# Kernel tuning notes

Hardware: AMD Instinct MI355X
Metric: run time of the kernel (lower is better)

Reference implementation:

```python
import jax, jax.numpy as jnp
import numpy as np

MOLS = 64
ATOMS = 256
N = MOLS * ATOMS
K_GB = 32
K_GNN = 16
HID = 128
OFFSET = 0.009            # GB dielectric offset (nm)
ALPHA, BETA, GAMMA = 1.0, 0.8, 4.85  # OBC2 coefficients
EPS_FACTOR = 138.935456   # Coulomb constant, kJ*nm/(mol*e^2)
PREF = -EPS_FACTOR * (1.0 - 1.0 / 78.5)


def _edges(key, k_neigh):
    # random intra-molecule neighbors, no self loops (mimics radius-graph structure)
    src = jnp.repeat(jnp.arange(N), k_neigh)
    off = jax.random.randint(key, (N * k_neigh,), 1, ATOMS)
    dst = (src // ATOMS) * ATOMS + (src % ATOMS + off) % ATOMS
    return jnp.stack([src, dst]).astype(jnp.int32)


def setup_inputs() -> dict:
    key = jax.random.key(0)
    ks = jax.random.split(key, 8)
    pos = (jax.random.uniform(ks[0], (N, 3), jnp.float32) * 1.5)
    q = jax.random.uniform(ks[1], (N, 1), jnp.float32) - 0.5
    rad = 0.15 + 0.05 * jax.random.uniform(ks[2], (N, 1), jnp.float32)
    scl = 0.8 + 0.2 * jax.random.uniform(ks[3], (N, 1), jnp.float32)
    rest = jax.random.uniform(ks[4], (N, 4), jnp.float32)
    atom_features = jnp.concatenate([q, rad, scl, rest], axis=1)
    batch = jnp.repeat(jnp.arange(MOLS), ATOMS).astype(jnp.int32)
    edge_index = _edges(ks[5], K_GB)
    gnn_edge_index = _edges(ks[6], K_GNN)

    def lin(k, fi, fo):
        return (jax.random.normal(k, (fi, fo), jnp.float32) / np.float32(np.sqrt(fi)),
                jnp.zeros((fo,), jnp.float32))
    kw = jax.random.split(ks[7], 6)
    i1_w1, i1_b1 = lin(kw[0], 2 * 2 + 1, HID)
    i1_w2, i1_b2 = lin(kw[1], HID, HID)
    i2_w1, i2_b1 = lin(kw[2], 2 * HID + 1, HID)
    i2_w2, i2_b2 = lin(kw[3], HID, HID)
    i3_w1, i3_b1 = lin(kw[4], 2 * HID + 1, HID)
    i3_w2, i3_b2 = lin(kw[5], HID, 1)
    return dict(pos=pos, atom_features=atom_features, batch=batch,
                edge_index=edge_index, gnn_edge_index=gnn_edge_index,
                i1_w1=i1_w1, i1_b1=i1_b1, i1_w2=i1_w2, i1_b2=i1_b2,
                i2_w1=i2_w1, i2_b1=i2_b1, i2_w2=i2_w2, i2_b2=i2_b2,
                i3_w1=i3_w1, i3_b1=i3_b1, i3_w2=i3_w2, i3_b2=i3_b2)


def _dist(pos, ei):
    d2 = jnp.sum((pos[ei[0]] - pos[ei[1]]) ** 2, axis=1)
    return jnp.sqrt(d2 + 1e-12)


def _gb_energies(pos, feats, ei):
    # GBNeck_interaction (Born radii via HCT descreening integral, OBC2 rescale)
    # followed by GBNeck_energies (pairwise GB + self energy), per-atom [N,1]
    n = pos.shape[0]
    src, dst = ei[0], ei[1]
    d = _dist(pos, ei)
    q, radius, scale = feats[:, 0], feats[:, 1], feats[:, 2]
    rho = radius - OFFSET
    sr_j = (scale * rho)[src]
    rho_i = rho[dst]
    U = d + sr_j
    L = jnp.maximum(rho_i, jnp.abs(d - sr_j))
    I = 0.5 * (1.0 / L - 1.0 / U
               + 0.25 * (d - sr_j ** 2 / d) * (1.0 / U ** 2 - 1.0 / L ** 2)
               + 0.5 * jnp.log(L / U) / d)
    I = jnp.where(rho_i < U, I, 0.0)
    Isum = jax.ops.segment_sum(I, dst, num_segments=n)
    psi = Isum * rho
    B = 1.0 / (1.0 / rho - jnp.tanh(ALPHA * psi - BETA * psi ** 2 + GAMMA * psi ** 3) / radius)
    Bi, Bj = B[dst], B[src]
    f_gb = jnp.sqrt(d ** 2 + Bi * Bj * jnp.exp(-d ** 2 / (4.0 * Bi * Bj)))
    e_pair = 0.5 * PREF * q[dst] * q[src] / f_gb  # 0.5: edges are double counted
    e = 0.5 * PREF * q ** 2 / B + jax.ops.segment_sum(e_pair, dst, num_segments=n)
    return e[:, None]


def _in_layer(x, ei, d, w1, b1, w2, b2):
    # IN_layer_all_swish_2pass: edge MLP on [x_i || x_j || d] + scatter-add
    n = x.shape[0]
    m = jnp.concatenate([x[ei[0]], x[ei[1]], d[:, None]], axis=1)
    h = jax.nn.silu(m @ w1 + b1)
    return jax.ops.segment_sum(h @ w2 + b2, ei[1], num_segments=n)


def _energies_all(pos, feats, ei, gei,
                  i1_w1, i1_b1, i1_w2, i1_b2,
                  i2_w1, i2_b1, i2_w2, i2_b2,
                  i3_w1, i3_b1, i3_w2, i3_b2):
    e_gb = _gb_energies(pos, feats, ei)
    d_gnn = _dist(pos, gei)
    x = jax.nn.silu(_in_layer(feats[:, :2], gei, d_gnn, i1_w1, i1_b1, i1_w2, i1_b2))
    x = jax.nn.silu(_in_layer(x, gei, d_gnn, i2_w1, i2_b1, i2_w2, i2_b2))
    x = _in_layer(x, gei, d_gnn, i3_w1, i3_b1, i3_w2, i3_b2)
    return e_gb + x


def reference(pos, atom_features, batch, edge_index, gnn_edge_index,
              i1_w1, i1_b1, i1_w2, i1_b2,
              i2_w1, i2_b1, i2_w2, i2_b2,
              i3_w1, i3_b1, i3_w2, i3_b2):
    ws = (i1_w1, i1_b1, i1_w2, i1_b2, i2_w1, i2_b1, i2_w2, i2_b2,
          i3_w1, i3_b1, i3_w2, i3_b2)
    efun = lambda p: _energies_all(p, atom_features, edge_index, gnn_edge_index, *ws)
    energies, vjp = jax.vjp(efun, pos)  # [N,1]
    (gpos,) = vjp(jnp.ones_like(energies))
    forces = -gpos
    energy = jax.ops.segment_sum(energies[:, 0], batch, num_segments=MOLS)[:, None]
    return energy, forces
```

## Files before the change

### kernel.cpp

```cpp
#include <hip/hip_runtime.h>
#include <hip/hip_bf16.h>

#define NATOMS 16384
#define MOLS   64
#define ATOMSM 256
#define EGB    524288
#define EGNN   262144
#define HID    128
#define NH     (NATOMS*HID)

#define OFFSETC 0.009f
#define ALPHAC  1.0f
#define BETAC   0.8f
#define GAMMAC  4.85f
#define PREFC   (-138.935456f*(1.0f-1.0f/78.5f))

typedef __hip_bfloat16 bf;
typedef __attribute__((ext_vector_type(8))) short bf8v;
typedef __attribute__((ext_vector_type(4))) float f4v;

__device__ __forceinline__ float b2f(bf x){ return __bfloat162float(x); }
__device__ __forceinline__ bf f2b(float x){ return __float2bfloat16(x); }
__device__ __forceinline__ short f2s(float x){ bf h = f2b(x); return *(short*)&h; }
__device__ __forceinline__ float s2f(short s){
    unsigned int x = ((unsigned int)(unsigned short)s) << 16;
    return __uint_as_float(x);
}
__device__ __forceinline__ float sigf(float x){ return 1.0f/(1.0f+__expf(-x)); }
__device__ __forceinline__ float waveRed(float v){
    v += __shfl_xor(v,32); v += __shfl_xor(v,16); v += __shfl_xor(v,8);
    v += __shfl_xor(v,4);  v += __shfl_xor(v,2);  v += __shfl_xor(v,1);
    return v;
}

__global__ __launch_bounds__(256) void k_gbA_dist(
    const float* __restrict__ pos, const float* __restrict__ feat,
    const int* __restrict__ ei, float* __restrict__ Isum,
    const int* __restrict__ gei, float* __restrict__ dgnn, int* __restrict__ cnt)
{
    int tid = threadIdx.x;
    if (blockIdx.x < 512){
        __shared__ float sPx[256], sPy[256], sPz[256], sRho[256], sSr[256];
        __shared__ float sI[256];
        int mbase = (blockIdx.x >> 3) * 256;
        {
            int i = mbase + tid;
            sPx[tid]=pos[3*i]; sPy[tid]=pos[3*i+1]; sPz[tid]=pos[3*i+2];
            float rad = feat[7*i+1], sc = feat[7*i+2];
            float rho = rad - OFFSETC;
            sRho[tid]=rho; sSr[tid]=sc*rho;
            sI[tid]=0.f;
        }
        __syncthreads();
        int T = blockIdx.x*256 + tid;
        int s = T >> 3, p = T & 7;
        int sl = s & 255;
        int e0 = s*32 + p*4;
        float px = sPx[sl], py = sPy[sl], pz = sPz[sl];
        float sr = sSr[sl];
        const int* dP = ei + EGB;
#pragma unroll
        for (int j=0;j<4;j++){
            int dl = dP[e0+j] & 255;
            float dx = px - sPx[dl];
            float dy = py - sPy[dl];
            float dz = pz - sPz[dl];
            float d  = sqrtf(dx*dx+dy*dy+dz*dz + 1e-12f);
            float rho_i = sRho[dl];
            float U = d + sr;
            if (rho_i < U){
                float L = fmaxf(rho_i, fabsf(d - sr));
                float invU = 1.0f/U, invL = 1.0f/L;
                float I = 0.5f*invL - 0.5f*invU
                        + 0.125f*(d - sr*sr/d)*(invU*invU - invL*invL)
                        + 0.25f*__logf(L*invU)/d;
                atomicAdd(&sI[dl], I);
            }
        }
        __syncthreads();
        atomicAdd(&Isum[mbase + tid], sI[tid]);
    } else {
        int e = (blockIdx.x-512)*256 + tid;
        if (e >= EGNN) return;
        int s = gei[e], dd = gei[EGNN+e];
        float dx = pos[3*s+0] - pos[3*dd+0];
        float dy = pos[3*s+1] - pos[3*dd+1];
        float dz = pos[3*s+2] - pos[3*dd+2];
        dgnn[e] = sqrtf(dx*dx+dy*dy+dz*dz + 1e-12f);
        atomicAdd(&cnt[dd], 1);
    }
}

__global__ __launch_bounds__(256) void k_gbB_scan(
    const float* __restrict__ feat, const float* __restrict__ Isum,
    float* __restrict__ Bv, float* __restrict__ cB, float* __restrict__ gB,
    float* __restrict__ egb,
    const int* __restrict__ cnt, int* __restrict__ rptr, int* __restrict__ cursor)
{
    int t = threadIdx.x;
    if (blockIdx.x < 64){
        int i = blockIdx.x*256 + t;
        float q   = feat[7*i+0];
        float rad = feat[7*i+1];
        float rho = rad - OFFSETC;
        float psi = Isum[i]*rho;
        float u = psi*(ALPHAC + psi*(-BETAC + GAMMAC*psi));
        float tt = tanhf(u);
        float B = 1.0f/(1.0f/rho - tt/rad);
        Bv[i] = B;
        float du = ALPHAC + psi*(-2.0f*BETAC + 3.0f*GAMMAC*psi);
        cB[i] = B*B*((1.0f-tt*tt)/rad)*du*rho;
        float Cs = 0.5f*PREFC*q*q;
        egb[i] = Cs/B;
        gB[i]  = -Cs/(B*B);
    } else {
        __shared__ int sc[256];
        int m = blockIdx.x - 64;
        int c = cnt[m*256+t];
        sc[t] = c; __syncthreads();
        for (int off=1; off<256; off<<=1){
            int x = (t>=off) ? sc[t-off] : 0;
            __syncthreads();
            sc[t] += x;
            __syncthreads();
        }
        int ex = m*4096 + sc[t] - c;
        rptr[m*256+t] = ex;
        cursor[m*256+t] = ex;
    }
}

__global__ __launch_bounds__(256) void k_gbC(
    const float* __restrict__ pos, const float* __restrict__ feat,
    const int* __restrict__ ei, const float* __restrict__ Bv,
    float* __restrict__ egb, float* __restrict__ gdgb, float* __restrict__ gB)
{
    __shared__ float sPx[256], sPy[256], sPz[256], sB[256], sQf[256];
    __shared__ float sE[256], sG[256];
    int tid = threadIdx.x;
    int mbase = (blockIdx.x >> 3) * 256;
    {
        int i = mbase + tid;
        sPx[tid]=pos[3*i]; sPy[tid]=pos[3*i+1]; sPz[tid]=pos[3*i+2];
        sB[tid]=Bv[i]; sQf[tid]=feat[7*i+0];
        sE[tid]=0.f; sG[tid]=0.f;
    }
    __syncthreads();
    int T = blockIdx.x*256 + tid;
    int s = T >> 3, p = T & 7;
    int sl = s & 255;
    int e0 = s*32 + p*4;
    float px = sPx[sl], py = sPy[sl], pz = sPz[sl];
    float qs = sQf[sl];
    float Bs = sB[sl];
    float gsrc = 0.f;
    const int* dP = ei + EGB;
#pragma unroll
    for (int j=0;j<4;j++){
        int dl = dP[e0+j] & 255;
        float dx = px - sPx[dl];
        float dy = py - sPy[dl];
        float dz = pz - sPz[dl];
        float d2 = dx*dx+dy*dy+dz*dz + 1e-12f;
        float d  = sqrtf(d2);
        float Bd = sB[dl];
        float C = 0.5f*PREFC*sQf[dl]*qs;
        float P = Bd*Bs;
        float ex = __expf(-d2/(4.f*P));
        float f2 = d2 + P*ex;
        float f  = sqrtf(f2);
        float f3i = 1.f/(f2*f);
        gdgb[e0+j] = -C*d*(1.f - 0.25f*ex)*f3i;
        float common = -C*ex*(1.f + d2/(4.f*P))*0.5f*f3i;
        atomicAdd(&sE[dl], C/f);
        atomicAdd(&sG[dl], common*Bs);
        gsrc += common*Bd;
    }
    gsrc += __shfl_xor(gsrc,1);
    gsrc += __shfl_xor(gsrc,2);
    gsrc += __shfl_xor(gsrc,4);
    if (p==0) atomicAdd(&sG[sl], gsrc);
    __syncthreads();
    atomicAdd(&egb[mbase + tid], sE[tid]);
    atomicAdd(&gB[mbase + tid],  sG[tid]);
}

__global__ __launch_bounds__(256) void k_gbE(
    const float* __restrict__ pos, const float* __restrict__ feat,
    const int* __restrict__ ei, const float* __restrict__ cB,
    const float* __restrict__ gB,
    const float* __restrict__ gdgb, float* __restrict__ grad)
{
    __shared__ float sPx[256], sPy[256], sPz[256], sRho[256], sSr[256], sCg[256];
    __shared__ float sGx[256], sGy[256], sGz[256];
    int tid = threadIdx.x;
    int mbase = (blockIdx.x >> 3) * 256;
    {
        int i = mbase + tid;
        sPx[tid]=pos[3*i]; sPy[tid]=pos[3*i+1]; sPz[tid]=pos[3*i+2];
        float rad = feat[7*i+1], sc = feat[7*i+2];
        float rho = rad - OFFSETC;
        sRho[tid]=rho; sSr[tid]=sc*rho;
        sCg[tid]=cB[i]*gB[i];
        sGx[tid]=0.f; sGy[tid]=0.f; sGz[tid]=0.f;
    }
    __syncthreads();
    int T = blockIdx.x*256 + tid;
    int s = T >> 3, p = T & 7;
    int sl = s & 255;
    int e0 = s*32 + p*4;
    float px = sPx[sl], py = sPy[sl], pz = sPz[sl];
    float sr = sSr[sl];
    float gx=0.f, gy=0.f, gz=0.f;
    const int* dP = ei + EGB;
#pragma unroll
    for (int j=0;j<4;j++){
        int dl = dP[e0+j] & 255;
        float dx = px - sPx[dl];
        float dy = py - sPy[dl];
        float dz = pz - sPz[dl];
        float d2 = dx*dx+dy*dy+dz*dz + 1e-12f;
        float d  = sqrtf(d2);
        float rho_i = sRho[dl];
        float U = d + sr;
        float gd = gdgb[e0+j];
        if (rho_i < U){
            float aa = fabsf(d - sr);
            float L, Lp;
            if (rho_i >= aa){ L = rho_i; Lp = 0.f; }
            else { L = aa; Lp = (d >= sr) ? 1.f : -1.f; }
            float invU = 1.f/U, invL = 1.f/L;
            float invU2=invU*invU, invL2=invL*invL;
            float dIdd = -0.5f*Lp*invL2 + 0.5f*invU2
                + 0.125f*(1.f + sr*sr/d2)*(invU2 - invL2)
                + 0.125f*(d - sr*sr/d)*(2.f*Lp*invL2*invL - 2.f*invU2*invU)
                + 0.25f*((Lp*invL - invU)/d - __logf(L*invU)/d2);
            gd += sCg[dl]*dIdd;
        }
        float c = gd/d;
        gx += c*dx; gy += c*dy; gz += c*dz;
        atomicAdd(&sGx[dl], -c*dx);
        atomicAdd(&sGy[dl], -c*dy);
        atomicAdd(&sGz[dl], -c*dz);
    }
    gx += __shfl_xor(gx,1); gx += __shfl_xor(gx,2); gx += __shfl_xor(gx,4);
    gy += __shfl_xor(gy,1); gy += __shfl_xor(gy,2); gy += __shfl_xor(gy,4);
    gz += __shfl_xor(gz,1); gz += __shfl_xor(gz,2); gz += __shfl_xor(gz,4);
    if (p==0){
        atomicAdd(&sGx[sl], gx);
        atomicAdd(&sGy[sl], gy);
        atomicAdd(&sGz[sl], gz);
    }
    __syncthreads();
    int i = mbase + tid;
    atomicAdd(&grad[3*i+0], sGx[tid]);
    atomicAdd(&grad[3*i+1], sGy[tid]);
    atomicAdd(&grad[3*i+2], sGz[tid]);
}

__global__ __launch_bounds__(256) void k_fill(
    const int* __restrict__ gei, int* __restrict__ cursor, int* __restrict__ csr)
{
    int e = blockIdx.x*256 + threadIdx.x;
    if (e >= EGNN) return;
    int dst = gei[EGNN+e];
    int pos = atomicAdd(&cursor[dst], 1);
    csr[pos] = e;
}

__global__ __launch_bounds__(256) void k_pre(
    const float* __restrict__ A2, const float* __restrict__ C1,
    const float* __restrict__ A3, const float* __restrict__ C2,
    short* __restrict__ C1t, short* __restrict__ C2t,
    short* __restrict__ A2at, short* __restrict__ A2bt,
    short* __restrict__ A3at, short* __restrict__ A3bt,
    short* __restrict__ rA2a, short* __restrict__ rA2b,
    short* __restrict__ rA3a, short* __restrict__ rA3b,
    short* __restrict__ rC1, short* __restrict__ rC2,
    const float* __restrict__ feat, const float* __restrict__ A1,
    bf* __restrict__ u1, bf* __restrict__ v1)
{
    if (blockIdx.x < 64){
        int gid = blockIdx.x*256 + threadIdx.x;
        int j = gid >> 7, k = gid & 127;
        C1t[gid]  = f2s(C1[k*HID+j]);
        C2t[gid]  = f2s(C2[k*HID+j]);
        A2at[gid] = f2s(A2[k*HID+j]);
        A2bt[gid] = f2s(A2[(HID+k)*HID+j]);
        A3at[gid] = f2s(A3[k*HID+j]);
        A3bt[gid] = f2s(A3[(HID+k)*HID+j]);
        rA2a[gid] = f2s(A2[gid]);
        rA2b[gid] = f2s(A2[HID*HID+gid]);
        rA3a[gid] = f2s(A3[gid]);
        rA3b[gid] = f2s(A3[HID*HID+gid]);
        rC1[gid]  = f2s(C1[gid]);
        rC2[gid]  = f2s(C2[gid]);
    } else {
        int gid = (blockIdx.x-64)*256 + threadIdx.x;
        int i = gid >> 7, k = gid & 127;
        float q = feat[7*i+0], r = feat[7*i+1];
        u1[gid] = f2b(q*A1[k]       + r*A1[HID+k]);
        v1[gid] = f2b(q*A1[2*HID+k] + r*A1[3*HID+k]);
    }
}

__global__ __launch_bounds__(128) void k_edge_fwd_dst(
    const int* __restrict__ csr, const int* __restrict__ rptr, const int* __restrict__ cnt,
    const float* __restrict__ dgnn, const bf* __restrict__ u, const bf* __restrict__ v,
    const float* __restrict__ wdp, const float* __restrict__ bb,
    bf* __restrict__ Hs, bf* __restrict__ dsO, bf* __restrict__ Sds)
{
    int dst = blockIdx.x, k = threadIdx.x;
    int n = cnt[dst], r0 = rptr[dst];
    float wd = wdp[k];
    float base = b2f(v[dst*HID+k]) + bb[k];
    float hsum = 0.f, dssum = 0.f;
    const short* us = (const short*)u;
    short* dso = (short*)dsO;
#pragma unroll 2
    for (int j=0;j<n;j++){
        int e = csr[r0+j];
        float a = s2f(us[(size_t)(e>>4)*HID + k]) + base + dgnn[e]*wd;
        float sg = sigf(a);
        hsum += a*sg;
        float dv = sg*(1.f + a*(1.f - sg));
        dssum += dv;
        dso[(size_t)e*HID + k] = f2s(dv);
    }
    Hs[dst*HID+k] = f2b(hsum);
    Sds[dst*HID+k] = f2b(dssum);
}

__global__ __launch_bounds__(256) void k_node_fwd_uv_mfma(
    const short* __restrict__ Hs, const int* __restrict__ cnt,
    const short* __restrict__ Ct, const float* __restrict__ D,
    const short* __restrict__ Aat, const short* __restrict__ Abt,
    bf* __restrict__ dsz, bf* __restrict__ u, bf* __restrict__ v)
{
    __shared__ short sx[64*HID];
    int lane = threadIdx.x & 63, w = threadIdx.x >> 6;
    int m0 = blockIdx.x*64 + w*16;
    int ar = lane & 15, kg = lane >> 4;
    bf8v af[4];
#pragma unroll
    for (int s=0;s<4;s++) af[s] = *(const bf8v*)&Hs[(size_t)(m0+ar)*HID + s*32 + kg*8];
    f4v acc[8];
#pragma unroll
    for (int nt=0;nt<8;nt++){
        acc[nt] = (f4v){0.f,0.f,0.f,0.f};
        const short* bp = Ct + (nt*16+ar)*HID + kg*8;
#pragma unroll
        for (int s=0;s<4;s++){
            bf8v bv = *(const bf8v*)(bp + s*32);
            acc[nt] = __builtin_amdgcn_mfma_f32_16x16x32_bf16(af[s], bv, acc[nt], 0,0,0);
        }
    }
    float cn[4];
#pragma unroll
    for (int r=0;r<4;r++) cn[r] = (float)cnt[m0 + kg*4 + r];
#pragma unroll
    for (int nt=0;nt<8;nt++){
        int j = nt*16 + ar;
        float Dj = D[j];
#pragma unroll
        for (int r=0;r<4;r++){
            int m = m0 + kg*4 + r;
            float zv = acc[nt][r] + cn[r]*Dj;
            float sg = sigf(zv);
            dsz[(size_t)m*HID + j] = f2b(sg*(1.f + zv*(1.f - sg)));
            sx[(w*16 + kg*4 + r)*HID + j] = f2s(zv*sg);
        }
    }
    __syncthreads();
#pragma unroll
    for (int s=0;s<4;s++) af[s] = *(const bf8v*)&sx[(w*16+ar)*HID + s*32 + kg*8];
    f4v au[8], av[8];
#pragma unroll
    for (int nt=0;nt<8;nt++){
        au[nt] = (f4v){0.f,0.f,0.f,0.f};
        av[nt] = (f4v){0.f,0.f,0.f,0.f};
        const short* bpa = Aat + (nt*16+ar)*HID + kg*8;
        const short* bpb = Abt + (nt*16+ar)*HID + kg*8;
#pragma unroll
        for (int s=0;s<4;s++){
            bf8v ba = *(const bf8v*)(bpa + s*32);
            bf8v bb = *(const bf8v*)(bpb + s*32);
            au[nt] = __builtin_amdgcn_mfma_f32_16x16x32_bf16(af[s], ba, au[nt], 0,0,0);
            av[nt] = __builtin_amdgcn_mfma_f32_16x16x32_bf16(af[s], bb, av[nt], 0,0,0);
        }
    }
#pragma unroll
    for (int nt=0;nt<8;nt++){
        int j = nt*16 + ar;
#pragma unroll
        for (int r=0;r<4;r++){
            int m = m0 + kg*4 + r;
            u[(size_t)m*HID + j] = f2b(au[nt][r]);
            v[(size_t)m*HID + j] = f2b(av[nt][r]);
        }
    }
}

__global__ __launch_bounds__(256) void k_gx_node_bwd_mfma(
    const short* __restrict__ Gs, const short* __restrict__ Gd,
    const short* __restrict__ gHin, const short* __restrict__ Sds,
    const short* __restrict__ Ra, const short* __restrict__ Rb,
    const bf* __restrict__ dsz, const short* __restrict__ Rc,
    bf* __restrict__ gHout)
{
    __shared__ short st[64*HID];
    int lane = threadIdx.x & 63, w = threadIdx.x >> 6;
    int m0 = blockIdx.x*64 + w*16;
    int ar = lane & 15, kg = lane >> 4;
    bf8v as_[4], ad_[4];
#pragma unroll
    for (int s=0;s<4;s++)
        as_[s] = *(const bf8v*)&Gs[(size_t)(m0+ar)*HID + s*32 + kg*8];
    if (Sds){
#pragma unroll
        for (int s=0;s<4;s++){
            bf8v g = *(const bf8v*)&gHin[(size_t)(m0+ar)*HID + s*32 + kg*8];
            bf8v sd = *(const bf8v*)&Sds[(size_t)(m0+ar)*HID + s*32 + kg*8];
            bf8v r;
#pragma unroll
            for (int i=0;i<8;i++) r[i] = f2s(s2f(g[i])*s2f(sd[i]));
            ad_[s] = r;
        }
    } else {
#pragma unroll
        for (int s=0;s<4;s++)
            ad_[s] = *(const bf8v*)&Gd[(size_t)(m0+ar)*HID + s*32 + kg*8];
    }
    f4v acc[8];
#pragma unroll
    for (int nt=0;nt<8;nt++){
        acc[nt] = (f4v){0.f,0.f,0.f,0.f};
        const short* bpa = Ra + (nt*16+ar)*HID + kg*8;
        const short* bpb = Rb + (nt*16+ar)*HID + kg*8;
#pragma unroll
        for (int s=0;s<4;s++){
            bf8v ba = *(const bf8v*)(bpa + s*32);
            bf8v bb = *(const bf8v*)(bpb + s*32);
            acc[nt] = __builtin_amdgcn_mfma_f32_16x16x32_bf16(as_[s], ba, acc[nt], 0,0,0);
            acc[nt] = __builtin_amdgcn_mfma_f32_16x16x32_bf16(ad_[s], bb, acc[nt], 0,0,0);
        }
    }
#pragma unroll
    for (int nt=0;nt<8;nt++){
        int j = nt*16 + ar;
#pragma unroll
        for (int r=0;r<4;r++){
            int m = m0 + kg*4 + r;
            float t = acc[nt][r] * b2f(dsz[(size_t)m*HID + j]);
            st[(w*16 + kg*4 + r)*HID + j] = f2s(t);
        }
    }
    __syncthreads();
    bf8v af[4];
#pragma unroll
    for (int s=0;s<4;s++) af[s] = *(const bf8v*)&st[(w*16+ar)*HID + s*32 + kg*8];
    f4v a2[8];
#pragma unroll
    for (int nt=0;nt<8;nt++){
        a2[nt] = (f4v){0.f,0.f,0.f,0.f};
        const short* bp = Rc + (nt*16+ar)*HID + kg*8;
#pragma unroll
        for (int s=0;s<4;s++){
            bf8v bc = *(const bf8v*)(bp + s*32);
            a2[nt] = __builtin_amdgcn_mfma_f32_16x16x32_bf16(af[s], bc, a2[nt], 0,0,0);
        }
    }
#pragma unroll
    for (int nt=0;nt<8;nt++){
        int j = nt*16 + ar;
#pragma unroll
        for (int r=0;r<4;r++){
            gHout[(size_t)(m0 + kg*4 + r)*HID + j] = f2b(a2[nt][r]);
        }
    }
}

__global__ __launch_bounds__(128) void k_l3_dst(
    const int* __restrict__ csr, const int* __restrict__ rptr, const int* __restrict__ cnt,
    const float* __restrict__ dgnn, const bf* __restrict__ u, const bf* __restrict__ v,
    const float* __restrict__ A3, const float* __restrict__ B3,
    const float* __restrict__ C3, const float* __restrict__ D3,
    bf* __restrict__ ds3, bf* __restrict__ Gd, float* __restrict__ x3)
{
    __shared__ float rr[2];
    int dst = blockIdx.x, k = threadIdx.x;
    int n = cnt[dst], r0 = rptr[dst];
    float wd = A3[256*HID+k], ck = C3[k];
    float base = b2f(v[dst*HID+k]) + B3[k];
    float hsum = 0.f, dssum = 0.f;
    const short* us = (const short*)u;
    short* dso = (short*)ds3;
#pragma unroll 2
    for (int j=0;j<n;j++){
        int e = csr[r0+j];
        float a = s2f(us[(size_t)(e>>4)*HID + k]) + base + dgnn[e]*wd;
        float sg = sigf(a);
        hsum += a*sg;
        float dv = sg*(1.f + a*(1.f - sg));
        dssum += dv;
        dso[(size_t)e*HID + k] = f2s(dv);
    }
    Gd[dst*HID+k] = f2b(ck*dssum);
    float pv = waveRed(ck*hsum);
    if ((k&63)==0) rr[k>>6] = pv;
    __syncthreads();
    if (k==0) x3[dst] = rr[0] + rr[1] + (float)n*D3[0];
}

__global__ __launch_bounds__(128) void k_l3_src(
    const bf* __restrict__ ds3,
    const float* __restrict__ A3, const float* __restrict__ C3,
    bf* __restrict__ Gs, float* __restrict__ gdg)
{
    __shared__ short sds[2048];
    __shared__ float sQ[16][130];
    int s = blockIdx.x, k = threadIdx.x;
    const bf8v* slab = (const bf8v*)((const short*)ds3 + (size_t)s*2048);
    ((bf8v*)sds)[k]     = slab[k];
    ((bf8v*)sds)[128+k] = slab[128+k];
    __syncthreads();
    float wd = A3[256*HID+k], ck = C3[k];
    float cw = ck*wd;
    float gs = 0.f;
#pragma unroll
    for (int t=0;t<16;t++){
        float dv = s2f(sds[t*128+k]);
        gs += dv;
        sQ[t][k] = dv*cw;
    }
    Gs[s*HID+k] = f2b(ck*gs);
    __syncthreads();
    int t = k >> 3, r = k & 7;
    float pg = 0.f;
#pragma unroll
    for (int i=0;i<16;i++) pg += sQ[t][i + 16*r];
    pg += __shfl_xor(pg,1); pg += __shfl_xor(pg,2); pg += __shfl_xor(pg,4);
    if (r==0) gdg[s*16+t] = pg;
}

__global__ __launch_bounds__(128) void k_bwd_src(
    const int* __restrict__ gei, const bf* __restrict__ ds2,
    const float* __restrict__ wdp, const bf* __restrict__ gH,
    bf* __restrict__ Gs, float* __restrict__ gdg)
{
    __shared__ short sds[2048];
    __shared__ short sgh[2048];
    __shared__ float sQ[16][130];
    int s = blockIdx.x, k = threadIdx.x;
    const bf8v* slab = (const bf8v*)((const short*)ds2 + (size_t)s*2048);
    ((bf8v*)sds)[k]     = slab[k];
    ((bf8v*)sds)[128+k] = slab[128+k];
    {
        int t = k >> 3, q = k & 7;
        int dst = gei[EGNN + s*16 + t];
        const bf8v* gr = (const bf8v*)((const short*)gH + (size_t)dst*HID);
        ((bf8v*)sgh)[t*16 + q*2]     = gr[q*2];
        ((bf8v*)sgh)[t*16 + q*2 + 1] = gr[q*2+1];
    }
    __syncthreads();
    float wd = wdp[k];
    float gs = 0.f;
#pragma unroll
    for (int t=0;t<16;t++){
        float ga = s2f(sgh[t*128+k]) * s2f(sds[t*128+k]);
        gs += ga;
        sQ[t][k] = ga*wd;
    }
    Gs[s*HID+k] = f2b(gs);
    __syncthreads();
    int t = k >> 3, r = k & 7;
    float pg = 0.f;
#pragma unroll
    for (int i=0;i<16;i++) pg += sQ[t][i + 16*r];
    pg += __shfl_xor(pg,1); pg += __shfl_xor(pg,2); pg += __shfl_xor(pg,4);
    if (r==0) gdg[s*16+t] += pg;
}

__global__ __launch_bounds__(128) void k_bwd1_src(
    const int* __restrict__ gei, const bf* __restrict__ ds1,
    const float* __restrict__ wdp, const bf* __restrict__ gH,
    float* __restrict__ gdg)
{
    __shared__ short sds[2048];
    __shared__ short sgh[2048];
    __shared__ float sQ[16][130];
    int s = blockIdx.x, k = threadIdx.x;
    const bf8v* slab = (const bf8v*)((const short*)ds1 + (size_t)s*2048);
    ((bf8v*)sds)[k]     = slab[k];
    ((bf8v*)sds)[128+k] = slab[128+k];
    {
        int t = k >> 3, q = k & 7;
        int dst = gei[EGNN + s*16 + t];
        const bf8v* gr = (const bf8v*)((const short*)gH + (size_t)dst*HID);
        ((bf8v*)sgh)[t*16 + q*2]     = gr[q*2];
        ((bf8v*)sgh)[t*16 + q*2 + 1] = gr[q*2+1];
    }
    __syncthreads();
    float wd = wdp[k];
#pragma unroll
    for (int t=0;t<16;t++){
        float ga = s2f(sgh[t*128+k]) * s2f(sds[t*128+k]);
        sQ[t][k] = ga*wd;
    }
    __syncthreads();
    int t = k >> 3, r = k & 7;
    float pg = 0.f;
#pragma unroll
    for (int i=0;i<16;i++) pg += sQ[t][i + 16*r];
    pg += __shfl_xor(pg,1); pg += __shfl_xor(pg,2); pg += __shfl_xor(pg,4);
    if (r==0) gdg[s*16+t] += pg;
}

__global__ __launch_bounds__(256) void k_force_atom(
    const float* __restrict__ pos, const int* __restrict__ gei,
    const int* __restrict__ csr, const int* __restrict__ rptr, const int* __restrict__ cnt,
    const float* __restrict__ dgnn, const float* __restrict__ gdg,
    const float* __restrict__ grad, float* __restrict__ fout)
{
    int T = blockIdx.x*256 + threadIdx.x;
    int i = T >> 3, p = T & 7;
    float px = pos[3*i+0], py = pos[3*i+1], pz = pos[3*i+2];
    float ax=0.f, ay=0.f, az=0.f;
    for (int j=p;j<16;j+=8){
        int e = i*16 + j;
        int o = gei[EGNN+e];
        float c = gdg[e]/dgnn[e];
        ax += c*(px - pos[3*o+0]);
        ay += c*(py - pos[3*o+1]);
        az += c*(pz - pos[3*o+2]);
    }
    int n = cnt[i], r0 = rptr[i];
    for (int j=p;j<n;j+=8){
        int e = csr[r0+j];
        int o = e >> 4;
        float c = gdg[e]/dgnn[e];
        ax += c*(px - pos[3*o+0]);
        ay += c*(py - pos[3*o+1]);
        az += c*(pz - pos[3*o+2]);
    }
    ax += __shfl_xor(ax,1); ax += __shfl_xor(ax,2); ax += __shfl_xor(ax,4);
    ay += __shfl_xor(ay,1); ay += __shfl_xor(ay,2); ay += __shfl_xor(ay,4);
    az += __shfl_xor(az,1); az += __shfl_xor(az,2); az += __shfl_xor(az,4);
    if (p==0){
        fout[3*i+0] = -(grad[3*i+0] + ax);
        fout[3*i+1] = -(grad[3*i+1] + ay);
        fout[3*i+2] = -(grad[3*i+2] + az);
    }
}

__global__ __launch_bounds__(256) void k_final(
    const float* __restrict__ egb, const float* __restrict__ x3,
    float* __restrict__ out)
{
    __shared__ float red[4];
    int m = blockIdx.x, tid = threadIdx.x;
    int i = m*ATOMSM + tid;
    float en = egb[i] + x3[i];
    float v = waveRed(en);
    int wave = tid>>6, lane = tid&63;
    if (lane==0) red[wave] = v;
    __syncthreads();
    if (tid==0) out[m] = red[0]+red[1]+red[2]+red[3];
}

extern "C" void kernel_launch(void* const* d_in, const int* in_sizes, int n_in,
                              void* d_out, int out_size, void* d_ws, size_t ws_size,
                              hipStream_t stream)
{
    const float* pos  = (const float*)d_in[0];
    const float* feat = (const float*)d_in[1];
    const int* ei  = (const int*)d_in[3];
    const int* gei = (const int*)d_in[4];
    const float* A1f = (const float*)d_in[5];  const float* B1f = (const float*)d_in[6];
    const float* C1f = (const float*)d_in[7];  const float* D1f = (const float*)d_in[8];
    const float* A2f = (const float*)d_in[9];  const float* B2f = (const float*)d_in[10];
    const float* C2f = (const float*)d_in[11]; const float* D2f = (const float*)d_in[12];
    const float* A3f = (const float*)d_in[13]; const float* B3f = (const float*)d_in[14];
    const float* C3f = (const float*)d_in[15]; const float* D3f = (const float*)d_in[16];

    float* w = (float*)d_ws;
    size_t off = 0;
    auto nxt = [&](size_t n)->float*{ float* p = w + off; off += (n + 255) & ~(size_t)255; return p; };
    float* Isum = nxt(NATOMS);
    int*   cnt  = (int*)nxt(NATOMS);
    float* grad = nxt(3*NATOMS);
    float* Bv = nxt(NATOMS); float* cB = nxt(NATOMS);
    float* gB = nxt(NATOMS); float* egb = nxt(NATOMS); float* x3 = nxt(NATOMS);
    int*   rptr = (int*)nxt(NATOMS);
    int*   curs = (int*)nxt(NATOMS);
    int*   csr  = (int*)nxt(EGNN);
    float* dgnn = nxt(EGNN); float* gdgnn = nxt(EGNN); float* gdgb = nxt(EGB);
    bf* dsz1 = (bf*)nxt(NH/2); bf* dsz2 = (bf*)nxt(NH/2);
    bf* Hs1 = (bf*)nxt(NH/2); bf* Hs2 = (bf*)nxt(NH/2);
    bf* Gs3 = (bf*)nxt(NH/2); bf* Gd3 = (bf*)nxt(NH/2);
    bf* Sds2 = (bf*)nxt(NH/2);
    bf* u1 = (bf*)nxt(NH/2); bf* v1 = (bf*)nxt(NH/2);
    bf* u2 = (bf*)nxt(NH/2); bf* v2 = (bf*)nxt(NH/2);
    bf* v3 = (bf*)nxt(NH/2);
    short* C1t  = (short*)nxt(8192); short* C2t  = (short*)nxt(8192);
    short* A2at = (short*)nxt(8192); short* A2bt = (short*)nxt(8192);
    short* A3at = (short*)nxt(8192); short* A3bt = (short*)nxt(8192);
    short* rA2a = (short*)nxt(8192); short* rA2b = (short*)nxt(8192);
    short* rA3a = (short*)nxt(8192); short* rA3b = (short*)nxt(8192);
    short* rC1  = (short*)nxt(8192); short* rC2  = (short*)nxt(8192);
    bf* ds1 = (bf*)nxt((size_t)EGNN*HID/2);
    bf* ds2 = (bf*)nxt((size_t)EGNN*HID/2);
    bf* ds3 = (bf*)nxt((size_t)EGNN*HID/2);
    bf* u3  = Hs1;
    bf* gH2 = Hs2;
    bf* Gs2 = Gs3;
    bf* gH1 = u3;

    hipMemsetAsync(Isum, 0, (size_t)5*NATOMS*sizeof(float), stream);

    k_pre<<<64+NH/256,256,0,stream>>>(A2f, C1f, A3f, C2f,
        C1t, C2t, A2at, A2bt, A3at, A3bt, rA2a, rA2b, rA3a, rA3b, rC1, rC2,
        feat, A1f, u1, v1);

    k_gbA_dist<<<512+EGNN/256,256,0,stream>>>(pos, feat, ei, Isum, gei, dgnn, cnt);
    k_gbB_scan<<<128,256,0,stream>>>(feat, Isum, Bv, cB, gB, egb, cnt, rptr, curs);
    k_fill<<<EGNN/256,256,0,stream>>>(gei, curs, csr);
    k_gbC<<<512,256,0,stream>>>(pos, feat, ei, Bv, egb, gdgb, gB);
    k_gbE<<<512,256,0,stream>>>(pos, feat, ei, cB, gB, gdgb, grad);

    k_edge_fwd_dst<<<NATOMS,128,0,stream>>>(csr, rptr, cnt, dgnn, u1, v1,
                                            A1f+4*HID, B1f, Hs1, ds1, Sds2 );
    k_node_fwd_uv_mfma<<<NATOMS/64,256,0,stream>>>((const short*)Hs1, cnt, C1t, D1f,
                                                   A2at, A2bt, dsz1, u2, v2);
    k_edge_fwd_dst<<<NATOMS,128,0,stream>>>(csr, rptr, cnt, dgnn, u2, v2,
                                            A2f+256*HID, B2f, Hs2, ds2, Sds2);
    k_node_fwd_uv_mfma<<<NATOMS/64,256,0,stream>>>((const short*)Hs2, cnt, C2t, D2f,
                                                   A3at, A3bt, dsz2, u3, v3);

    k_l3_dst<<<NATOMS,128,0,stream>>>(csr, rptr, cnt, dgnn, u3, v3,
                                      A3f, B3f, C3f, D3f, ds3, Gd3, x3);
    k_l3_src<<<NATOMS,128,0,stream>>>(ds3, A3f, C3f, Gs3, gdgnn);

    k_gx_node_bwd_mfma<<<NATOMS/64,256,0,stream>>>((const short*)Gs3, (const short*)Gd3,
        (const short*)nullptr, (const short*)nullptr, rA3a, rA3b, dsz2, rC2, gH2);
    k_bwd_src<<<NATOMS,128,0,stream>>>(gei, ds2, A2f+256*HID, gH2, Gs2, gdgnn);
    k_gx_node_bwd_mfma<<<NATOMS/64,256,0,stream>>>((const short*)Gs2, (const short*)nullptr,
        (const short*)gH2, (const short*)Sds2, rA2a, rA2b, dsz1, rC1, gH1);
    k_bwd1_src<<<NATOMS,128,0,stream>>>(gei, ds1, A1f+4*HID, gH1, gdgnn);

    k_force_atom<<<NATOMS*8/256,256,0,stream>>>(pos, gei, csr, rptr, cnt, dgnn, gdgnn,
                                                grad, (float*)d_out + MOLS);
    k_final<<<MOLS,256,0,stream>>>(egb, x3, (float*)d_out);
}
```

Before: 381.9 us.

## Recompute per-edge SiLU derivatives in backward instead of storing ds tensors

The forward edge kernels no longer write the per-edge, per-channel SiLU derivative arrays (three EGNN×128 bf16 buffers). The source-side backward kernels instead gather v rows for the 16 destinations, read u and dgnn, and recompute the pre-activation and its derivative. This trades about 64 MB of writes and reads per layer for extra sigmoid arithmetic and gathered v loads. u3 gets its own buffer because it must now stay alive into the backward pass.

```diff
diff --git a/kernel.cpp b/kernel.cpp
--- a/kernel.cpp
+++ b/kernel.cpp
@@ -308,7 +308,7 @@
     const int* __restrict__ csr, const int* __restrict__ rptr, const int* __restrict__ cnt,
     const float* __restrict__ dgnn, const bf* __restrict__ u, const bf* __restrict__ v,
     const float* __restrict__ wdp, const float* __restrict__ bb,
-    bf* __restrict__ Hs, bf* __restrict__ dsO, bf* __restrict__ Sds)
+    bf* __restrict__ Hs, bf* __restrict__ Sds)
 {
     int dst = blockIdx.x, k = threadIdx.x;
     int n = cnt[dst], r0 = rptr[dst];
@@ -316,16 +316,13 @@
     float base = b2f(v[dst*HID+k]) + bb[k];
     float hsum = 0.f, dssum = 0.f;
     const short* us = (const short*)u;
-    short* dso = (short*)dsO;
 #pragma unroll 2
     for (int j=0;j<n;j++){
         int e = csr[r0+j];
         float a = s2f(us[(size_t)(e>>4)*HID + k]) + base + dgnn[e]*wd;
         float sg = sigf(a);
         hsum += a*sg;
-        float dv = sg*(1.f + a*(1.f - sg));
-        dssum += dv;
-        dso[(size_t)e*HID + k] = f2s(dv);
+        dssum += sg*(1.f + a*(1.f - sg));
     }
     Hs[dst*HID+k] = f2b(hsum);
     Sds[dst*HID+k] = f2b(dssum);
@@ -485,7 +482,7 @@
     const float* __restrict__ dgnn, const bf* __restrict__ u, const bf* __restrict__ v,
     const float* __restrict__ A3, const float* __restrict__ B3,
     const float* __restrict__ C3, const float* __restrict__ D3,
-    bf* __restrict__ ds3, bf* __restrict__ Gd, float* __restrict__ x3)
+    bf* __restrict__ Gd, float* __restrict__ x3)
 {
     __shared__ float rr[2];
     int dst = blockIdx.x, k = threadIdx.x;
@@ -494,16 +491,13 @@
     float base = b2f(v[dst*HID+k]) + B3[k];
     float hsum = 0.f, dssum = 0.f;
     const short* us = (const short*)u;
-    short* dso = (short*)ds3;
 #pragma unroll 2
     for (int j=0;j<n;j++){
         int e = csr[r0+j];
         float a = s2f(us[(size_t)(e>>4)*HID + k]) + base + dgnn[e]*wd;
         float sg = sigf(a);
         hsum += a*sg;
-        float dv = sg*(1.f + a*(1.f - sg));
-        dssum += dv;
-        dso[(size_t)e*HID + k] = f2s(dv);
+        dssum += sg*(1.f + a*(1.f - sg));
     }
     Gd[dst*HID+k] = f2b(ck*dssum);
     float pv = waveRed(ck*hsum);
@@ -513,23 +507,33 @@
 }
 
 __global__ __launch_bounds__(128) void k_l3_src(
-    const bf* __restrict__ ds3,
-    const float* __restrict__ A3, const float* __restrict__ C3,
+    const int* __restrict__ gei, const float* __restrict__ dgnn,
+    const bf* __restrict__ u, const bf* __restrict__ v,
+    const float* __restrict__ A3, const float* __restrict__ B3,
+    const float* __restrict__ C3,
     bf* __restrict__ Gs, float* __restrict__ gdg)
 {
-    __shared__ short sds[2048];
+    __shared__ short sv[2048];
     __shared__ float sQ[16][130];
     int s = blockIdx.x, k = threadIdx.x;
-    const bf8v* slab = (const bf8v*)((const short*)ds3 + (size_t)s*2048);
-    ((bf8v*)sds)[k]     = slab[k];
-    ((bf8v*)sds)[128+k] = slab[128+k];
-    __syncthreads();
-    float wd = A3[256*HID+k], ck = C3[k];
+    {
+        int t = k >> 3, q = k & 7;
+        int dst = gei[EGNN + s*16 + t];
+        const bf8v* vr = (const bf8v*)((const short*)v + (size_t)dst*HID);
+        ((bf8v*)sv)[t*16 + q*2]     = vr[q*2];
+        ((bf8v*)sv)[t*16 + q*2 + 1] = vr[q*2+1];
+    }
+    __syncthreads();
+    float uk = b2f(u[s*HID+k]);
+    float wd = A3[256*HID+k], bk = B3[k], ck = C3[k];
     float cw = ck*wd;
     float gs = 0.f;
+    const float* dgp = dgnn + s*16;
 #pragma unroll
     for (int t=0;t<16;t++){
-        float dv = s2f(sds[t*128+k]);
+        float a = uk + s2f(sv[t*128+k]) + dgp[t]*wd + bk;
+        float sg = sigf(a);
+        float dv = sg*(1.f + a*(1.f - sg));
         gs += dv;
         sQ[t][k] = dv*cw;
     }
@@ -544,30 +548,37 @@
 }
 
 __global__ __launch_bounds__(128) void k_bwd_src(
-    const int* __restrict__ gei, const bf* __restrict__ ds2,
-    const float* __restrict__ wdp, const bf* __restrict__ gH,
+    const int* __restrict__ gei, const float* __restrict__ dgnn,
+    const bf* __restrict__ u, const bf* __restrict__ v,
+    const float* __restrict__ wdp, const float* __restrict__ bb,
+    const bf* __restrict__ gH,
     bf* __restrict__ Gs, float* __restrict__ gdg)
 {
-    __shared__ short sds[2048];
+    __shared__ short sv[2048];
     __shared__ short sgh[2048];
     __shared__ float sQ[16][130];
     int s = blockIdx.x, k = threadIdx.x;
-    const bf8v* slab = (const bf8v*)((const short*)ds2 + (size_t)s*2048);
-    ((bf8v*)sds)[k]     = slab[k];
-    ((bf8v*)sds)[128+k] = slab[128+k];
     {
         int t = k >> 3, q = k & 7;
         int dst = gei[EGNN + s*16 + t];
+        const bf8v* vr = (const bf8v*)((const short*)v + (size_t)dst*HID);
         const bf8v* gr = (const bf8v*)((const short*)gH + (size_t)dst*HID);
+        ((bf8v*)sv)[t*16 + q*2]      = vr[q*2];
+        ((bf8v*)sv)[t*16 + q*2 + 1]  = vr[q*2+1];
         ((bf8v*)sgh)[t*16 + q*2]     = gr[q*2];
         ((bf8v*)sgh)[t*16 + q*2 + 1] = gr[q*2+1];
     }
     __syncthreads();
-    float wd = wdp[k];
+    float uk = b2f(u[s*HID+k]);
+    float wd = wdp[k], bk = bb[k];
     float gs = 0.f;
+    const float* dgp = dgnn + s*16;
 #pragma unroll
     for (int t=0;t<16;t++){
-        float ga = s2f(sgh[t*128+k]) * s2f(sds[t*128+k]);
+        float a = uk + s2f(sv[t*128+k]) + dgp[t]*wd + bk;
+        float sg = sigf(a);
+        float dv = sg*(1.f + a*(1.f - sg));
+        float ga = s2f(sgh[t*128+k]) * dv;
         gs += ga;
         sQ[t][k] = ga*wd;
     }
@@ -582,30 +593,35 @@
 }
 
 __global__ __launch_bounds__(128) void k_bwd1_src(
-    const int* __restrict__ gei, const bf* __restrict__ ds1,
-    const float* __restrict__ wdp, const bf* __restrict__ gH,
-    float* __restrict__ gdg)
-{
-    __shared__ short sds[2048];
+    const int* __restrict__ gei, const float* __restrict__ dgnn,
+    const bf* __restrict__ u, const bf* __restrict__ v,
+    const float* __restrict__ wdp, const float* __restrict__ bb,
+    const bf* __restrict__ gH, float* __restrict__ gdg)
+{
+    __shared__ short sv[2048];
     __shared__ short sgh[2048];
     __shared__ float sQ[16][130];
     int s = blockIdx.x, k = threadIdx.x;
-    const bf8v* slab = (const bf8v*)((const short*)ds1 + (size_t)s*2048);
-    ((bf8v*)sds)[k]     = slab[k];
-    ((bf8v*)sds)[128+k] = slab[128+k];
     {
         int t = k >> 3, q = k & 7;
         int dst = gei[EGNN + s*16 + t];
+        const bf8v* vr = (const bf8v*)((const short*)v + (size_t)dst*HID);
         const bf8v* gr = (const bf8v*)((const short*)gH + (size_t)dst*HID);
+        ((bf8v*)sv)[t*16 + q*2]      = vr[q*2];
+        ((bf8v*)sv)[t*16 + q*2 + 1]  = vr[q*2+1];
         ((bf8v*)sgh)[t*16 + q*2]     = gr[q*2];
         ((bf8v*)sgh)[t*16 + q*2 + 1] = gr[q*2+1];
     }
     __syncthreads();
-    float wd = wdp[k];
+    float uk = b2f(u[s*HID+k]);
+    float wd = wdp[k], bk = bb[k];
+    const float* dgp = dgnn + s*16;
 #pragma unroll
     for (int t=0;t<16;t++){
-        float ga = s2f(sgh[t*128+k]) * s2f(sds[t*128+k]);
-        sQ[t][k] = ga*wd;
+        float a = uk + s2f(sv[t*128+k]) + dgp[t]*wd + bk;
+        float sg = sigf(a);
+        float dv = sg*(1.f + a*(1.f - sg));
+        sQ[t][k] = s2f(sgh[t*128+k]) * dv * wd;
     }
     __syncthreads();
     int t = k >> 3, r = k & 7;
@@ -701,20 +717,16 @@
     bf* Sds2 = (bf*)nxt(NH/2);
     bf* u1 = (bf*)nxt(NH/2); bf* v1 = (bf*)nxt(NH/2);
     bf* u2 = (bf*)nxt(NH/2); bf* v2 = (bf*)nxt(NH/2);
-    bf* v3 = (bf*)nxt(NH/2);
+    bf* u3 = (bf*)nxt(NH/2); bf* v3 = (bf*)nxt(NH/2);
     short* C1t  = (short*)nxt(8192); short* C2t  = (short*)nxt(8192);
     short* A2at = (short*)nxt(8192); short* A2bt = (short*)nxt(8192);
     short* A3at = (short*)nxt(8192); short* A3bt = (short*)nxt(8192);
     short* rA2a = (short*)nxt(8192); short* rA2b = (short*)nxt(8192);
     short* rA3a = (short*)nxt(8192); short* rA3b = (short*)nxt(8192);
     short* rC1  = (short*)nxt(8192); short* rC2  = (short*)nxt(8192);
-    bf* ds1 = (bf*)nxt((size_t)EGNN*HID/2);
-    bf* ds2 = (bf*)nxt((size_t)EGNN*HID/2);
-    bf* ds3 = (bf*)nxt((size_t)EGNN*HID/2);
-    bf* u3  = Hs1;
     bf* gH2 = Hs2;
     bf* Gs2 = Gs3;
-    bf* gH1 = u3;
+    bf* gH1 = Hs1;
 
     hipMemsetAsync(Isum, 0, (size_t)5*NATOMS*sizeof(float), stream);
 
@@ -729,24 +741,25 @@
     k_gbE<<<512,256,0,stream>>>(pos, feat, ei, cB, gB, gdgb, grad);
 
     k_edge_fwd_dst<<<NATOMS,128,0,stream>>>(csr, rptr, cnt, dgnn, u1, v1,
-                                            A1f+4*HID, B1f, Hs1, ds1, Sds2 );
+                                            A1f+4*HID, B1f, Hs1, Sds2 );
     k_node_fwd_uv_mfma<<<NATOMS/64,256,0,stream>>>((const short*)Hs1, cnt, C1t, D1f,
                                                    A2at, A2bt, dsz1, u2, v2);
     k_edge_fwd_dst<<<NATOMS,128,0,stream>>>(csr, rptr, cnt, dgnn, u2, v2,
-                                            A2f+256*HID, B2f, Hs2, ds2, Sds2);
+                                            A2f+256*HID, B2f, Hs2, Sds2);
     k_node_fwd_uv_mfma<<<NATOMS/64,256,0,stream>>>((const short*)Hs2, cnt, C2t, D2f,
                                                    A3at, A3bt, dsz2, u3, v3);
 
     k_l3_dst<<<NATOMS,128,0,stream>>>(csr, rptr, cnt, dgnn, u3, v3,
-                                      A3f, B3f, C3f, D3f, ds3, Gd3, x3);
-    k_l3_src<<<NATOMS,128,0,stream>>>(ds3, A3f, C3f, Gs3, gdgnn);
+                                      A3f, B3f, C3f, D3f, Gd3, x3);
+    k_l3_src<<<NATOMS,128,0,stream>>>(gei, dgnn, u3, v3, A3f, B3f, C3f, Gs3, gdgnn);
 
     k_gx_node_bwd_mfma<<<NATOMS/64,256,0,stream>>>((const short*)Gs3, (const short*)Gd3,
         (const short*)nullptr, (const short*)nullptr, rA3a, rA3b, dsz2, rC2, gH2);
-    k_bwd_src<<<NATOMS,128,0,stream>>>(gei, ds2, A2f+256*HID, gH2, Gs2, gdgnn);
+    k_bwd_src<<<NATOMS,128,0,stream>>>(gei, dgnn, u2, v2, A2f+256*HID, B2f, gH2,
+                                       Gs2, gdgnn);
     k_gx_node_bwd_mfma<<<NATOMS/64,256,0,stream>>>((const short*)Gs2, (const short*)nullptr,
         (const short*)gH2, (const short*)Sds2, rA2a, rA2b, dsz1, rC1, gH1);
-    k_bwd1_src<<<NATOMS,128,0,stream>>>(gei, ds1, A1f+4*HID, gH1, gdgnn);
+    k_bwd1_src<<<NATOMS,128,0,stream>>>(gei, dgnn, u1, v1, A1f+4*HID, B1f, gH1, gdgnn);
 
     k_force_atom<<<NATOMS*8/256,256,0,stream>>>(pos, gei, csr, rptr, cnt, dgnn, gdgnn,
                                                 grad, (float*)d_out + MOLS);
```

After: 386.4 us. Within noise of the previous version (+1.2%).
